# Performance work log

Measured on AMD Instinct MI355X. Metric: run time of the kernel, lower is better.

Reference implementation:

```python
import jax, jax.numpy as jnp
import numpy as np


def setup_inputs() -> dict:
    key = jax.random.key(0)
    k1, k2, k3, k4, k5 = jax.random.split(key, 5)
    B, S, ENC, DEC = 32, 2048, 1024, 512
    hidden = jax.random.normal(k1, (B, DEC), dtype=jnp.float32)
    encoder_outputs = jax.random.normal(k2, (B, S, ENC), dtype=jnp.float32)
    W = jax.random.normal(k3, (DEC, ENC + DEC), dtype=jnp.float32) * (1.0 / np.sqrt(ENC + DEC))
    b = jax.random.normal(k4, (DEC,), dtype=jnp.float32) * 0.01
    v = jax.random.uniform(k5, (DEC,), dtype=jnp.float32)  # torch.rand init
    return {"hidden": hidden, "encoder_outputs": encoder_outputs, "W": W, "b": b, "v": v}


def reference(hidden, encoder_outputs, W, b, v):
    # hidden: [B, D_dec], encoder_outputs: [B, S, D_enc]
    # Concat order in original: (hidden, encoder_outputs) -> split W accordingly.
    D_dec = hidden.shape[-1]
    Wh = W[:, :D_dec]   # [D_dec, D_dec] acts on hidden
    We = W[:, D_dec:]   # [D_dec, D_enc] acts on encoder_outputs
    # energy: tanh(Linear(cat(hidden_repeated, enc))) == tanh(h@Wh^T + enc@We^T + b)
    h_proj = jnp.einsum('bd,ed->be', hidden, Wh)                 # [B, D_dec]
    e_proj = jnp.einsum('bse,de->bsd', encoder_outputs, We)      # [B, S, D_dec]
    energy = jnp.tanh(e_proj + h_proj[:, None, :] + b)           # [B, S, D_dec]
    # scores: v . energy per (b, s); softmax over src_len
    scores = jnp.einsum('d,bsd->bs', v, energy)                  # [B, S]
    attn = jax.nn.softmax(scores, axis=-1)
    return attn[:, None, :]                                       # [B, 1, S]
```

## Files before the change

kernel.cpp:

```cpp
#include <hip/hip_runtime.h>
#include <hip/hip_bf16.h>


typedef __attribute__((ext_vector_type(8))) short bf16x8;
typedef __attribute__((ext_vector_type(4))) float f32x4;

__device__ __forceinline__ ushort f2bf(float x) {
    __hip_bfloat16 h = __float2bfloat16(x);
    return *reinterpret_cast<ushort*>(&h);
}

#define WS_WBF   0
#define WS_HB    (1u << 20)
#define WS_SCORE ((1u << 20) + (64u << 10))

__global__ void convert_we(const float* __restrict__ W, ushort* __restrict__ Wbf) {
    int idx = blockIdx.x * 256 + threadIdx.x;
    int d  = idx >> 8;
    int e4 = (idx & 255) * 4;
    float4 f = *(const float4*)(W + (size_t)d * 1536 + 512 + e4);
    ushort4 u;
    u.x = f2bf(f.x); u.y = f2bf(f.y); u.z = f2bf(f.z); u.w = f2bf(f.w);
    *(ushort4*)(Wbf + (size_t)d * 1024 + e4) = u;
}

__global__ void hproj_kernel(const float* __restrict__ hidden,
                             const float* __restrict__ W,
                             const float* __restrict__ bias,
                             float* __restrict__ hb) {
    int idx = blockIdx.x * 256 + threadIdx.x;
    int b = idx >> 9, d = idx & 511;
    const float4* hp = (const float4*)(hidden + b * 512);
    const float4* wp = (const float4*)(W + (size_t)d * 1536);
    float acc = 0.f;
#pragma unroll 8
    for (int j = 0; j < 128; ++j) {
        float4 h = hp[j], w = wp[j];
        acc += h.x * w.x + h.y * w.y + h.z * w.z + h.w * w.w;
    }
    hb[idx] = acc + bias[d];
}

__launch_bounds__(256, 2)
__global__ void eproj_scores(const float* __restrict__ enc,
                             const ushort* __restrict__ Wbf,
                             const float* __restrict__ hb,
                             const float* __restrict__ v,
                             float* __restrict__ scores) {
    __shared__ ushort Alds[64 * 72];
    __shared__ float  spart[4][64];

    const int tid = threadIdx.x;
    const int l  = tid & 63, w = tid >> 6;
    const int q  = l >> 4,  ln = l & 15;
    const long m0 = (long)blockIdx.x * 64;
    const int  nbase = w * 128;

    f32x4 acc[4][8];
#pragma unroll
    for (int mt = 0; mt < 4; ++mt)
#pragma unroll
        for (int nt = 0; nt < 8; ++nt)
            acc[mt][nt] = (f32x4){0.f, 0.f, 0.f, 0.f};

    for (int kt = 0; kt < 1024; kt += 64) {
        __syncthreads();
#pragma unroll
        for (int i = 0; i < 4; ++i) {
            int idx = tid + 256 * i;
            int row = idx >> 4, ch = idx & 15;
            float4 f = *(const float4*)(enc + (m0 + row) * 1024 + kt + ch * 4);
            ushort4 u;
            u.x = f2bf(f.x); u.y = f2bf(f.y); u.z = f2bf(f.z); u.w = f2bf(f.w);
            *(ushort4*)(&Alds[row * 72 + ch * 4]) = u;
        }
        __syncthreads();
#pragma unroll
        for (int ks = 0; ks < 64; ks += 32) {
            bf16x8 af[4];
#pragma unroll
            for (int mt = 0; mt < 4; ++mt)
                af[mt] = *(bf16x8*)(&Alds[(ln + 16 * mt) * 72 + ks + q * 8]);
#pragma unroll
            for (int nt = 0; nt < 8; ++nt) {
                int n = nbase + nt * 16 + ln;
                bf16x8 bfr = *(const bf16x8*)(Wbf + (size_t)n * 1024 + kt + ks + q * 8);
#pragma unroll
                for (int mt = 0; mt < 4; ++mt)
                    acc[mt][nt] = __builtin_amdgcn_mfma_f32_16x16x32_bf16(
                        af[mt], bfr, acc[mt][nt], 0, 0, 0);
            }
        }
    }

    const int bidx = (int)(m0 >> 11);
    float partial[4][4];
#pragma unroll
    for (int mt = 0; mt < 4; ++mt)
#pragma unroll
        for (int r = 0; r < 4; ++r) partial[mt][r] = 0.f;

#pragma unroll
    for (int nt = 0; nt < 8; ++nt) {
        int d = nbase + nt * 16 + ln;
        float hbv = hb[bidx * 512 + d];
        float vv  = v[d];
#pragma unroll
        for (int mt = 0; mt < 4; ++mt)
#pragma unroll
            for (int r = 0; r < 4; ++r) {
                float x = acc[mt][nt][r] + hbv;
                float e = __expf(2.f * x);
                partial[mt][r] += vv * (1.f - 2.f / (e + 1.f));
            }
    }
#pragma unroll
    for (int mt = 0; mt < 4; ++mt)
#pragma unroll
        for (int r = 0; r < 4; ++r) {
            float s = partial[mt][r];
            s += __shfl_xor(s, 1);
            s += __shfl_xor(s, 2);
            s += __shfl_xor(s, 4);
            s += __shfl_xor(s, 8);
            partial[mt][r] = s;
        }
    if (ln == 0) {
#pragma unroll
        for (int mt = 0; mt < 4; ++mt)
#pragma unroll
            for (int r = 0; r < 4; ++r)
                spart[w][mt * 16 + q * 4 + r] = partial[mt][r];
    }
    __syncthreads();
    if (tid < 64) {
        float s = spart[0][tid] + spart[1][tid] + spart[2][tid] + spart[3][tid];
        scores[m0 + tid] = s;
    }
}

__global__ void softmax_kernel(const float* __restrict__ scores, float* __restrict__ out) {
    int b = blockIdx.x;
    const float* sc = scores + b * 2048;
    __shared__ float wred[4], wsum[4];

    float lmax = -1e30f;
    for (int i = threadIdx.x; i < 2048; i += 256) lmax = fmaxf(lmax, sc[i]);
#pragma unroll
    for (int m = 1; m < 64; m <<= 1) lmax = fmaxf(lmax, __shfl_xor(lmax, m));
    if ((threadIdx.x & 63) == 0) wred[threadIdx.x >> 6] = lmax;
    __syncthreads();
    float gmax = fmaxf(fmaxf(wred[0], wred[1]), fmaxf(wred[2], wred[3]));

    float lsum = 0.f;
    for (int i = threadIdx.x; i < 2048; i += 256) lsum += __expf(sc[i] - gmax);
#pragma unroll
    for (int m = 1; m < 64; m <<= 1) lsum += __shfl_xor(lsum, m);
    if ((threadIdx.x & 63) == 0) wsum[threadIdx.x >> 6] = lsum;
    __syncthreads();
    float inv = 1.f / (wsum[0] + wsum[1] + wsum[2] + wsum[3]);

    for (int i = threadIdx.x; i < 2048; i += 256)
        out[b * 2048 + i] = __expf(sc[i] - gmax) * inv;
}

extern "C" void kernel_launch(void* const* d_in, const int* in_sizes, int n_in,
                              void* d_out, int out_size, void* d_ws, size_t ws_size,
                              hipStream_t stream) {
    const float* hidden = (const float*)d_in[0];
    const float* enc    = (const float*)d_in[1];
    const float* W      = (const float*)d_in[2];
    const float* bias   = (const float*)d_in[3];
    const float* v      = (const float*)d_in[4];
    float* out = (float*)d_out;

    char* ws = (char*)d_ws;
    ushort* Wbf   = (ushort*)(ws + WS_WBF);
    float*  hb    = (float*)(ws + WS_HB);
    float*  score = (float*)(ws + WS_SCORE);

    hipLaunchKernelGGL(convert_we,   dim3(512),  dim3(256), 0, stream, W, Wbf);
    hipLaunchKernelGGL(hproj_kernel, dim3(64),   dim3(256), 0, stream, hidden, W, bias, hb);
    hipLaunchKernelGGL(eproj_scores, dim3(1024), dim3(256), 0, stream, enc, Wbf, hb, v, score);
    hipLaunchKernelGGL(softmax_kernel, dim3(32), dim3(256), 0, stream, score, out);
}
```

Measured before the change: 495.9 us.

## Double-buffer encoder tiles via async global-to-LDS loads with swizzled fp32 staging

The encoder tile is now staged as fp32 directly from global memory into LDS with global_load_lds, double-buffered so the next K-slab loads while the current one feeds MFMA. The conversion to bf16 moves to the LDS read, and an XOR swizzle is meant to avoid bank conflicts. The M tile shrinks from 64 to 32 rows, so the grid doubles and launch bounds rise to 3 waves per SIMD for better occupancy, and W fragments are prefetched into registers for the whole K step. In exchange, W is read twice as often per output row and the LDS footprint in fp32 is larger.

Result: slower. 605.5 us (+22.1%).

```diff
diff --git a/kernel.cpp b/kernel.cpp
--- a/kernel.cpp
+++ b/kernel.cpp
@@ -8,6 +8,15 @@
 __device__ __forceinline__ ushort f2bf(float x) {
     __hip_bfloat16 h = __float2bfloat16(x);
     return *reinterpret_cast<ushort*>(&h);
+}
+
+__device__ __forceinline__ bf16x8 pack8(float4 a, float4 b) {
+    bf16x8 o;
+    o[0] = (short)f2bf(a.x); o[1] = (short)f2bf(a.y);
+    o[2] = (short)f2bf(a.z); o[3] = (short)f2bf(a.w);
+    o[4] = (short)f2bf(b.x); o[5] = (short)f2bf(b.y);
+    o[6] = (short)f2bf(b.z); o[7] = (short)f2bf(b.w);
+    return o;
 }
 
 #define WS_WBF   0
@@ -41,62 +50,94 @@
     hb[idx] = acc + bias[d];
 }
 
-__launch_bounds__(256, 2)
+__launch_bounds__(256, 3)
 __global__ void eproj_scores(const float* __restrict__ enc,
                              const ushort* __restrict__ Wbf,
                              const float* __restrict__ hb,
                              const float* __restrict__ v,
                              float* __restrict__ scores) {
-    __shared__ ushort Alds[64 * 72];
-    __shared__ float  spart[4][64];
-
-    const int tid = threadIdx.x;
-    const int l  = tid & 63, w = tid >> 6;
-    const int q  = l >> 4,  ln = l & 15;
-    const long m0 = (long)blockIdx.x * 64;
-    const int  nbase = w * 128;
-
-    f32x4 acc[4][8];
-#pragma unroll
-    for (int mt = 0; mt < 4; ++mt)
+    __shared__ float Abuf[2][32 * 64];
+    __shared__ float spart[4][32];
+
+    const int tid  = threadIdx.x;
+    const int lane = tid & 63, w = tid >> 6;
+    const int q    = lane >> 4, ln = lane & 15;
+    const long m0  = (long)blockIdx.x * 32;
+    const int bidx = (int)(m0 >> 11);
+    const int nbase = w * 128;
+
+    f32x4 acc[2][8];
+#pragma unroll
+    for (int mt = 0; mt < 2; ++mt)
 #pragma unroll
         for (int nt = 0; nt < 8; ++nt)
             acc[mt][nt] = (f32x4){0.f, 0.f, 0.f, 0.f};
 
+#pragma unroll
+    for (int rr = 0; rr < 2; ++rr) {
+        int p = rr * 256 + tid;
+        int r = p >> 4;
+        int c = (p & 15) ^ (r & 15);
+        const float* g = enc + (m0 + r) * 1024 + c * 4;
+        float* lb = &Abuf[0][(rr * 256 + w * 64) * 4];
+        __builtin_amdgcn_global_load_lds(
+            (const __attribute__((address_space(1))) void*)g,
+            (__attribute__((address_space(3))) void*)lb, 16, 0, 0);
+    }
+
+    int buf = 0;
     for (int kt = 0; kt < 1024; kt += 64) {
+        bf16x8 bfr[2][8];
+#pragma unroll
+        for (int ks2 = 0; ks2 < 2; ++ks2)
+#pragma unroll
+            for (int nt = 0; nt < 8; ++nt)
+                bfr[ks2][nt] = *(const bf16x8*)(
+                    Wbf + (size_t)(nbase + nt * 16 + ln) * 1024 + kt + ks2 * 32 + q * 8);
+
         __syncthreads();
-#pragma unroll
-        for (int i = 0; i < 4; ++i) {
-            int idx = tid + 256 * i;
-            int row = idx >> 4, ch = idx & 15;
-            float4 f = *(const float4*)(enc + (m0 + row) * 1024 + kt + ch * 4);
-            ushort4 u;
-            u.x = f2bf(f.x); u.y = f2bf(f.y); u.z = f2bf(f.z); u.w = f2bf(f.w);
-            *(ushort4*)(&Alds[row * 72 + ch * 4]) = u;
-        }
-        __syncthreads();
-#pragma unroll
-        for (int ks = 0; ks < 64; ks += 32) {
-            bf16x8 af[4];
-#pragma unroll
-            for (int mt = 0; mt < 4; ++mt)
-                af[mt] = *(bf16x8*)(&Alds[(ln + 16 * mt) * 72 + ks + q * 8]);
-#pragma unroll
-            for (int nt = 0; nt < 8; ++nt) {
-                int n = nbase + nt * 16 + ln;
-                bf16x8 bfr = *(const bf16x8*)(Wbf + (size_t)n * 1024 + kt + ks + q * 8);
-#pragma unroll
-                for (int mt = 0; mt < 4; ++mt)
-                    acc[mt][nt] = __builtin_amdgcn_mfma_f32_16x16x32_bf16(
-                        af[mt], bfr, acc[mt][nt], 0, 0, 0);
+
+        if (kt + 64 < 1024) {
+#pragma unroll
+            for (int rr = 0; rr < 2; ++rr) {
+                int p = rr * 256 + tid;
+                int r = p >> 4;
+                int c = (p & 15) ^ (r & 15);
+                const float* g = enc + (m0 + r) * 1024 + (kt + 64) + c * 4;
+                float* lb = &Abuf[buf ^ 1][(rr * 256 + w * 64) * 4];
+                __builtin_amdgcn_global_load_lds(
+                    (const __attribute__((address_space(1))) void*)g,
+                    (__attribute__((address_space(3))) void*)lb, 16, 0, 0);
             }
         }
-    }
-
-    const int bidx = (int)(m0 >> 11);
-    float partial[4][4];
-#pragma unroll
-    for (int mt = 0; mt < 4; ++mt)
+
+        const float* lcur = Abuf[buf];
+#pragma unroll
+        for (int ks2 = 0; ks2 < 2; ++ks2) {
+            bf16x8 af[2];
+#pragma unroll
+            for (int mt = 0; mt < 2; ++mt) {
+                int r  = ln + 16 * mt;
+                int cb = ks2 * 8 + 2 * q;
+                int pA = r * 16 + ( cb      ^ (r & 15));
+                int pB = r * 16 + ((cb + 1) ^ (r & 15));
+                float4 a0 = *(const float4*)(lcur + pA * 4);
+                float4 a1 = *(const float4*)(lcur + pB * 4);
+                af[mt] = pack8(a0, a1);
+            }
+#pragma unroll
+            for (int nt = 0; nt < 8; ++nt)
+#pragma unroll
+                for (int mt = 0; mt < 2; ++mt)
+                    acc[mt][nt] = __builtin_amdgcn_mfma_f32_16x16x32_bf16(
+                        af[mt], bfr[ks2][nt], acc[mt][nt], 0, 0, 0);
+        }
+        buf ^= 1;
+    }
+
+    float partial[2][4];
+#pragma unroll
+    for (int mt = 0; mt < 2; ++mt)
 #pragma unroll
         for (int r = 0; r < 4; ++r) partial[mt][r] = 0.f;
 
@@ -106,7 +147,7 @@
         float hbv = hb[bidx * 512 + d];
         float vv  = v[d];
 #pragma unroll
-        for (int mt = 0; mt < 4; ++mt)
+        for (int mt = 0; mt < 2; ++mt)
 #pragma unroll
             for (int r = 0; r < 4; ++r) {
                 float x = acc[mt][nt][r] + hbv;
@@ -115,7 +156,7 @@
             }
     }
 #pragma unroll
-    for (int mt = 0; mt < 4; ++mt)
+    for (int mt = 0; mt < 2; ++mt)
 #pragma unroll
         for (int r = 0; r < 4; ++r) {
             float s = partial[mt][r];
@@ -127,13 +168,13 @@
         }
     if (ln == 0) {
 #pragma unroll
-        for (int mt = 0; mt < 4; ++mt)
+        for (int mt = 0; mt < 2; ++mt)
 #pragma unroll
             for (int r = 0; r < 4; ++r)
                 spart[w][mt * 16 + q * 4 + r] = partial[mt][r];
     }
     __syncthreads();
-    if (tid < 64) {
+    if (tid < 32) {
         float s = spart[0][tid] + spart[1][tid] + spart[2][tid] + spart[3][tid];
         scores[m0 + tid] = s;
     }
@@ -181,6 +222,6 @@
 
     hipLaunchKernelGGL(convert_we,   dim3(512),  dim3(256), 0, stream, W, Wbf);
     hipLaunchKernelGGL(hproj_kernel, dim3(64),   dim3(256), 0, stream, hidden, W, bias, hb);
-    hipLaunchKernelGGL(eproj_scores, dim3(1024), dim3(256), 0, stream, enc, Wbf, hb, v, score);
+    hipLaunchKernelGGL(eproj_scores, dim3(2048), dim3(256), 0, stream, enc, Wbf, hb, v, score);
     hipLaunchKernelGGL(softmax_kernel, dim3(32), dim3(256), 0, stream, score, out);
 }
```

## Double-buffer fp32 encoder tiles via direct-to-LDS loads and split N across blocks

Applied to the files above, without the earlier changes.

Restructures the main GEMM kernel. Encoder tiles are loaded as fp32 straight into swizzled, double-buffered LDS with global_load_lds and converted to bf16 at fragment-read time, while W fragments are prefetched into registers one step ahead. Each block now covers 128 rows by 128 columns, so N is split over four blocks, and partial scores are combined with atomicAdd into a buffer zeroed by a fused prep kernel that also absorbs the W conversion and the hidden projection. The aims are overlapping loads with MFMA and raising occupancy, at the cost of reading each encoder row four times (once per N block) and adding float atomics, which make the summation order nondeterministic.

After: 508.5 us. 1.03x slower.

```diff
diff --git a/kernel.cpp b/kernel.cpp
--- a/kernel.cpp
+++ b/kernel.cpp
@@ -10,90 +10,144 @@
     return *reinterpret_cast<ushort*>(&h);
 }
 
+__device__ __forceinline__ bf16x8 pack8(float4 a, float4 b) {
+    bf16x8 o;
+    o[0] = (short)f2bf(a.x); o[1] = (short)f2bf(a.y);
+    o[2] = (short)f2bf(a.z); o[3] = (short)f2bf(a.w);
+    o[4] = (short)f2bf(b.x); o[5] = (short)f2bf(b.y);
+    o[6] = (short)f2bf(b.z); o[7] = (short)f2bf(b.w);
+    return o;
+}
+
 #define WS_WBF   0
 #define WS_HB    (1u << 20)
 #define WS_SCORE ((1u << 20) + (64u << 10))
 
-__global__ void convert_we(const float* __restrict__ W, ushort* __restrict__ Wbf) {
-    int idx = blockIdx.x * 256 + threadIdx.x;
-    int d  = idx >> 8;
-    int e4 = (idx & 255) * 4;
-    float4 f = *(const float4*)(W + (size_t)d * 1536 + 512 + e4);
-    ushort4 u;
-    u.x = f2bf(f.x); u.y = f2bf(f.y); u.z = f2bf(f.z); u.w = f2bf(f.w);
-    *(ushort4*)(Wbf + (size_t)d * 1024 + e4) = u;
-}
-
-__global__ void hproj_kernel(const float* __restrict__ hidden,
-                             const float* __restrict__ W,
-                             const float* __restrict__ bias,
-                             float* __restrict__ hb) {
-    int idx = blockIdx.x * 256 + threadIdx.x;
-    int b = idx >> 9, d = idx & 511;
-    const float4* hp = (const float4*)(hidden + b * 512);
-    const float4* wp = (const float4*)(W + (size_t)d * 1536);
-    float acc = 0.f;
+__global__ void prep_kernel(const float* __restrict__ W,
+                            const float* __restrict__ hidden,
+                            const float* __restrict__ bias,
+                            ushort* __restrict__ Wbf,
+                            float* __restrict__ hb,
+                            float* __restrict__ score) {
+    const int bid = blockIdx.x, tid = threadIdx.x;
+    if (bid < 512) {
+        int idx = bid * 256 + tid;
+        int d  = idx >> 8;
+        int e4 = (idx & 255) * 4;
+        float4 f = *(const float4*)(W + (size_t)d * 1536 + 512 + e4);
+        ushort4 u;
+        u.x = f2bf(f.x); u.y = f2bf(f.y); u.z = f2bf(f.z); u.w = f2bf(f.w);
+        *(ushort4*)(Wbf + (size_t)d * 1024 + e4) = u;
+    } else if (bid < 576) {
+        int idx = (bid - 512) * 256 + tid;
+        int b = idx >> 9, d = idx & 511;
+        const float4* hp = (const float4*)(hidden + b * 512);
+        const float4* wp = (const float4*)(W + (size_t)d * 1536);
+        float acc = 0.f;
 #pragma unroll 8
-    for (int j = 0; j < 128; ++j) {
-        float4 h = hp[j], w = wp[j];
-        acc += h.x * w.x + h.y * w.y + h.z * w.z + h.w * w.w;
-    }
-    hb[idx] = acc + bias[d];
-}
-
-__launch_bounds__(256, 2)
+        for (int j = 0; j < 128; ++j) {
+            float4 h = hp[j], w = wp[j];
+            acc += h.x * w.x + h.y * w.y + h.z * w.z + h.w * w.w;
+        }
+        hb[idx] = acc + bias[d];
+    } else {
+        int idx = (bid - 576) * 256 + tid;
+        float4 z = {0.f, 0.f, 0.f, 0.f};
+        *(float4*)(score + (size_t)idx * 4) = z;
+    }
+}
+
+__launch_bounds__(256, 3)
 __global__ void eproj_scores(const float* __restrict__ enc,
                              const ushort* __restrict__ Wbf,
                              const float* __restrict__ hb,
                              const float* __restrict__ v,
                              float* __restrict__ scores) {
-    __shared__ ushort Alds[64 * 72];
-    __shared__ float  spart[4][64];
-
-    const int tid = threadIdx.x;
-    const int l  = tid & 63, w = tid >> 6;
-    const int q  = l >> 4,  ln = l & 15;
-    const long m0 = (long)blockIdx.x * 64;
-    const int  nbase = w * 128;
-
-    f32x4 acc[4][8];
+    __shared__ alignas(16) float Abuf[2][128 * 32];
+    __shared__ float spart[2][128];
+
+    const int tid  = threadIdx.x;
+    const int lane = tid & 63, w = tid >> 6;
+    const int wm = w >> 1, wn = w & 1;
+    const int q = lane >> 4, ln = lane & 15;
+    const int  nblk = blockIdx.x & 3;
+    const long m0   = (long)(blockIdx.x >> 2) * 128;
+    const int  bidx = (int)(m0 >> 11);
+    const int  n0   = nblk * 128 + wn * 64;
+
+    f32x4 acc[4][4];
 #pragma unroll
     for (int mt = 0; mt < 4; ++mt)
 #pragma unroll
-        for (int nt = 0; nt < 8; ++nt)
+        for (int nt = 0; nt < 4; ++nt)
             acc[mt][nt] = (f32x4){0.f, 0.f, 0.f, 0.f};
 
-    for (int kt = 0; kt < 1024; kt += 64) {
+    const ushort* bptr[4];
+#pragma unroll
+    for (int nt = 0; nt < 4; ++nt)
+        bptr[nt] = Wbf + (size_t)(n0 + nt * 16 + ln) * 1024 + q * 8;
+
+    int sA0[4], sA1[4];
+#pragma unroll
+    for (int mt = 0; mt < 4; ++mt) {
+        int rA = wm * 64 + mt * 16 + ln;
+        sA0[mt] = (rA * 8 + ((2 * q)     ^ (rA & 7))) * 4;
+        sA1[mt] = (rA * 8 + ((2 * q + 1) ^ (rA & 7))) * 4;
+    }
+
+#pragma unroll
+    for (int i = 0; i < 4; ++i) {
+        int s = i * 256 + tid;
+        int r = s >> 3;
+        int c = (s & 7) ^ (r & 7);
+        const float* g = enc + (m0 + r) * 1024 + c * 4;
+        float* lb = &Abuf[0][(i * 256 + w * 64) * 4];
+        __builtin_amdgcn_global_load_lds(
+            (const __attribute__((address_space(1))) void*)g,
+            (__attribute__((address_space(3))) void*)lb, 16, 0, 0);
+    }
+    bf16x8 bfr[2][4];
+#pragma unroll
+    for (int nt = 0; nt < 4; ++nt)
+        bfr[0][nt] = *(const bf16x8*)(bptr[nt]);
+
+    int buf = 0;
+#pragma unroll 2
+    for (int kt = 0; kt < 32; ++kt) {
+        const int p = kt & 1;
         __syncthreads();
-#pragma unroll
-        for (int i = 0; i < 4; ++i) {
-            int idx = tid + 256 * i;
-            int row = idx >> 4, ch = idx & 15;
-            float4 f = *(const float4*)(enc + (m0 + row) * 1024 + kt + ch * 4);
-            ushort4 u;
-            u.x = f2bf(f.x); u.y = f2bf(f.y); u.z = f2bf(f.z); u.w = f2bf(f.w);
-            *(ushort4*)(&Alds[row * 72 + ch * 4]) = u;
-        }
-        __syncthreads();
-#pragma unroll
-        for (int ks = 0; ks < 64; ks += 32) {
-            bf16x8 af[4];
-#pragma unroll
-            for (int mt = 0; mt < 4; ++mt)
-                af[mt] = *(bf16x8*)(&Alds[(ln + 16 * mt) * 72 + ks + q * 8]);
-#pragma unroll
-            for (int nt = 0; nt < 8; ++nt) {
-                int n = nbase + nt * 16 + ln;
-                bf16x8 bfr = *(const bf16x8*)(Wbf + (size_t)n * 1024 + kt + ks + q * 8);
-#pragma unroll
-                for (int mt = 0; mt < 4; ++mt)
-                    acc[mt][nt] = __builtin_amdgcn_mfma_f32_16x16x32_bf16(
-                        af[mt], bfr, acc[mt][nt], 0, 0, 0);
+
+        if (kt < 31) {
+#pragma unroll
+            for (int i = 0; i < 4; ++i) {
+                int s = i * 256 + tid;
+                int r = s >> 3;
+                int c = (s & 7) ^ (r & 7);
+                const float* g = enc + (m0 + r) * 1024 + (kt + 1) * 32 + c * 4;
+                float* lb = &Abuf[buf ^ 1][(i * 256 + w * 64) * 4];
+                __builtin_amdgcn_global_load_lds(
+                    (const __attribute__((address_space(1))) void*)g,
+                    (__attribute__((address_space(3))) void*)lb, 16, 0, 0);
             }
-        }
-    }
-
-    const int bidx = (int)(m0 >> 11);
+#pragma unroll
+            for (int nt = 0; nt < 4; ++nt)
+                bfr[p ^ 1][nt] = *(const bf16x8*)(bptr[nt] + (size_t)(kt + 1) * 32);
+        }
+
+        const float* Ab = Abuf[buf];
+#pragma unroll
+        for (int mt = 0; mt < 4; ++mt) {
+            float4 a0 = *(const float4*)(Ab + sA0[mt]);
+            float4 a1 = *(const float4*)(Ab + sA1[mt]);
+            bf16x8 af = pack8(a0, a1);
+#pragma unroll
+            for (int nt = 0; nt < 4; ++nt)
+                acc[mt][nt] = __builtin_amdgcn_mfma_f32_16x16x32_bf16(
+                    af, bfr[p][nt], acc[mt][nt], 0, 0, 0);
+        }
+        buf ^= 1;
+    }
+
     float partial[4][4];
 #pragma unroll
     for (int mt = 0; mt < 4; ++mt)
@@ -101,8 +155,8 @@
         for (int r = 0; r < 4; ++r) partial[mt][r] = 0.f;
 
 #pragma unroll
-    for (int nt = 0; nt < 8; ++nt) {
-        int d = nbase + nt * 16 + ln;
+    for (int nt = 0; nt < 4; ++nt) {
+        int d = n0 + nt * 16 + ln;
         float hbv = hb[bidx * 512 + d];
         float vv  = v[d];
 #pragma unroll
@@ -130,13 +184,11 @@
         for (int mt = 0; mt < 4; ++mt)
 #pragma unroll
             for (int r = 0; r < 4; ++r)
-                spart[w][mt * 16 + q * 4 + r] = partial[mt][r];
+                spart[wn][wm * 64 + mt * 16 + q * 4 + r] = partial[mt][r];
     }
     __syncthreads();
-    if (tid < 64) {
-        float s = spart[0][tid] + spart[1][tid] + spart[2][tid] + spart[3][tid];
-        scores[m0 + tid] = s;
-    }
+    if (tid < 128)
+        atomicAdd(&scores[m0 + tid], spart[0][tid] + spart[1][tid]);
 }
 
 __global__ void softmax_kernel(const float* __restrict__ scores, float* __restrict__ out) {
@@ -179,8 +231,9 @@
     float*  hb    = (float*)(ws + WS_HB);
     float*  score = (float*)(ws + WS_SCORE);
 
-    hipLaunchKernelGGL(convert_we,   dim3(512),  dim3(256), 0, stream, W, Wbf);
-    hipLaunchKernelGGL(hproj_kernel, dim3(64),   dim3(256), 0, stream, hidden, W, bias, hb);
-    hipLaunchKernelGGL(eproj_scores, dim3(1024), dim3(256), 0, stream, enc, Wbf, hb, v, score);
+    hipLaunchKernelGGL(prep_kernel,  dim3(640),  dim3(256), 0, stream,
+                       W, hidden, bias, Wbf, hb, score);
+    hipLaunchKernelGGL(eproj_scores, dim3(2048), dim3(256), 0, stream,
+                       enc, Wbf, hb, v, score);
     hipLaunchKernelGGL(softmax_kernel, dim3(32), dim3(256), 0, stream, score, out);
 }
```
